# Optimization experiments

Hardware: AMD Instinct MI355X
Metric: run time of the kernel (lower is better)

Reference implementation:

```python
import jax, jax.numpy as jnp
import numpy as np

B, N, D, H, F = 16, 512, 768, 12, 3072
HD = D // H
EPS = 1e-5
NEG_INF = -1e30  # stand-in for -inf; softmax of all -inf rows handled via nan_to_num semantics


def layer_norm(x, g, b):
    mu = jnp.mean(x, axis=-1, keepdims=True)
    var = jnp.mean(jnp.square(x - mu), axis=-1, keepdims=True)
    return (x - mu) * jax.lax.rsqrt(var + EPS) * g + b


def setup_inputs() -> dict:
    key = jax.random.key(0)
    ks = jax.random.split(key, 16)
    s = 0.02
    return {
        "x": jax.random.normal(ks[0], (B, N, D), jnp.float32),
        "spatial_encoding": jax.random.normal(ks[1], (B, N, N), jnp.float32),
        "edge_encoding": jax.random.normal(ks[2], (B, N, N), jnp.float32),
        "Wq": jax.random.normal(ks[3], (D, D), jnp.float32) * s,
        "Wk": jax.random.normal(ks[4], (D, D), jnp.float32) * s,
        "Wv": jax.random.normal(ks[5], (D, D), jnp.float32) * s,
        "bv": jnp.zeros((D,), jnp.float32),
        "Wo": jax.random.normal(ks[6], (D, D), jnp.float32) * s,
        "bo": jnp.zeros((D,), jnp.float32),
        "g1": jnp.ones((D,), jnp.float32),
        "be1": jnp.zeros((D,), jnp.float32),
        "g2": jnp.ones((D,), jnp.float32),
        "be2": jnp.zeros((D,), jnp.float32),
        "W1": jax.random.normal(ks[7], (D, F), jnp.float32) * s,
        "bf1": jnp.zeros((F,), jnp.float32),
        "W2": jax.random.normal(ks[8], (F, D), jnp.float32) * s,
        "bf2": jnp.zeros((D,), jnp.float32),
    }


def reference(x, spatial_encoding, edge_encoding, Wq, Wk, Wv, bv, Wo, bo,
              g1, be1, g2, be2, W1, bf1, W2, bf2):
    scale = D ** (-0.5)
    h = layer_norm(x, g1, be1)                              # n1(x)
    bias = (spatial_encoding + edge_encoding)[:, None]      # [B,1,N,N]

    q = (h @ Wq).reshape(B, N, H, HD).transpose(0, 2, 1, 3)  # [B,H,N,hd]
    k = (h @ Wk).reshape(B, N, H, HD).transpose(0, 2, 1, 3)
    v = (h @ Wv + bv).reshape(B, N, H, HD).transpose(0, 2, 1, 3)

    a = jnp.einsum('bhqd,bhkd->bhqk', q, k) * scale + bias   # [B,H,N,N]
    # pad rows (all-zero score rows) get -inf -> softmax NaN -> nan_to_num -> 0
    row_nonzero = jnp.any(a != 0, axis=-1, keepdims=True)
    a = jnp.where(row_nonzero, a, NEG_INF)
    p = jax.nn.softmax(a, axis=-1)
    p = jnp.where(row_nonzero, p, 0.0)  # mirrors nan_to_num on all -inf rows

    o = jnp.einsum('bhqk,bhkd->bhqd', p, v)                  # [B,H,N,hd]
    o = o.transpose(0, 2, 1, 3).reshape(B, N, D)
    att_output = o @ Wo + bo + x                              # residual

    pad_mask = jnp.any(att_output == 0, axis=-1)              # [B,N]
    ffn_in = layer_norm(x, g2, be2)                           # note: n2(x), as in source
    hmid = jax.nn.gelu(ffn_in @ W1 + bf1, approximate=True)
    ffn_out = hmid @ W2 + bf2 + att_output
    return jnp.where(pad_mask[..., None], 0.0, ffn_out)
```

## Files before the change

### kernel.cpp

```cpp
#include <hip/hip_runtime.h>
#include <math.h>

typedef unsigned short u16;
typedef __bf16 bf16x8 __attribute__((ext_vector_type(8)));
typedef float f32x4 __attribute__((ext_vector_type(4)));

__device__ __forceinline__ u16 f2bf(float f){
  union{float f; unsigned u;} v; v.f = f;
  return (u16)((v.u + 0x7fffu + ((v.u >> 16) & 1u)) >> 16);
}
__device__ __forceinline__ float bf2f(u16 b){
  union{unsigned u; float f;} v; v.u = (unsigned)b << 16; return v.f;
}

#define LOG2E 1.4426950408889634f

__global__ void prep_weights(const float* __restrict__ Wq, const float* __restrict__ Wk,
                             const float* __restrict__ Wv, const float* __restrict__ Wo,
                             const float* __restrict__ W1, const float* __restrict__ W2,
                             const float* __restrict__ g1, const float* __restrict__ g2,
                             u16* __restrict__ WqkvT, u16* __restrict__ WoT,
                             u16* __restrict__ W1T, u16* __restrict__ W2T, float qscale){
  __shared__ float t[32][33];
  int bid = blockIdx.x;
  const float* src; u16* dst; const float* rs; float sc; int R, C, bx, by;
  if (bid < 576)      {            src=Wq; dst=WqkvT;          rs=g1;      sc=qscale; R=768;  C=768;  bx=bid%24; by=bid/24; }
  else if (bid <1152) { bid-=576;  src=Wk; dst=WqkvT+768*768;  rs=g1;      sc=1.f;    R=768;  C=768;  bx=bid%24; by=bid/24; }
  else if (bid <1728) { bid-=1152; src=Wv; dst=WqkvT+1536*768; rs=g1;      sc=1.f;    R=768;  C=768;  bx=bid%24; by=bid/24; }
  else if (bid <2304) { bid-=1728; src=Wo; dst=WoT;            rs=nullptr; sc=1.f;    R=768;  C=768;  bx=bid%24; by=bid/24; }
  else if (bid <4608) { bid-=2304; src=W1; dst=W1T;            rs=g2;      sc=1.f;    R=768;  C=3072; bx=bid%96; by=bid/96; }
  else                { bid-=4608; src=W2; dst=W2T;            rs=nullptr; sc=1.f;    R=3072; C=768;  bx=bid%24; by=bid/24; }
  int c0 = bx * 32, r0 = by * 32;
  int tx = threadIdx.x, ty = threadIdx.y;
  #pragma unroll
  for (int i = 0; i < 4; i++)
    t[ty + i*8][tx] = src[(size_t)(r0 + ty + i*8) * C + c0 + tx];
  __syncthreads();
  float fac = (rs ? rs[r0 + tx] : 1.f) * sc;
  #pragma unroll
  for (int i = 0; i < 4; i++)
    dst[(size_t)(c0 + ty + i*8) * R + r0 + tx] = f2bf(t[tx][ty + i*8] * fac);
}

__global__ __launch_bounds__(256) void fold_bias(
    const float* __restrict__ Wq, const float* __restrict__ Wk,
    const float* __restrict__ Wv, const float* __restrict__ W1,
    const float* __restrict__ be1, const float* __restrict__ be2,
    const float* __restrict__ bv, const float* __restrict__ bf1,
    float* __restrict__ qkvb, float* __restrict__ bf1f){
  __shared__ float red[4][64];
  int tx = threadIdx.x & 63, ty = threadIdx.x >> 6;
  int j = blockIdx.x * 64 + tx;
  const float* W; int col, stride; const float* bvec;
  if (j < 768)       { W = Wq; col = j;        stride = 768;  bvec = be1; }
  else if (j < 1536) { W = Wk; col = j - 768;  stride = 768;  bvec = be1; }
  else if (j < 2304) { W = Wv; col = j - 1536; stride = 768;  bvec = be1; }
  else               { W = W1; col = j - 2304; stride = 3072; bvec = be2; }
  float s = 0.f;
  for (int k = ty * 192; k < (ty + 1) * 192; k++)
    s += bvec[k] * W[(size_t)k * stride + col];
  red[ty][tx] = s;
  __syncthreads();
  if (ty == 0){
    s = red[0][tx] + red[1][tx] + red[2][tx] + red[3][tx];
    if (j < 1536)      qkvb[j] = s;
    else if (j < 2304) qkvb[j] = s + bv[col];
    else               bf1f[col] = s + bf1[col];
  }
}

__global__ void bias_prep(u16* __restrict__ dst, const float* __restrict__ sp,
                          const float* __restrict__ ed){
  int t = blockIdx.x * blockDim.x + threadIdx.x;
  int row = t >> 7, c0 = (t & 127) * 4;
  size_t base = (size_t)row * 512;
  float4 s = *(const float4*)&sp[base + c0];
  float4 e = *(const float4*)&ed[base + c0];
  int kt = c0 >> 7, cw = c0 & 127, fk = cw >> 4, l0 = cw & 15;
  u16* o = dst + base + kt*128 + fk;
  o[(l0+0)*8] = f2bf((s.x+e.x)*LOG2E);
  o[(l0+1)*8] = f2bf((s.y+e.y)*LOG2E);
  o[(l0+2)*8] = f2bf((s.z+e.z)*LOG2E);
  o[(l0+3)*8] = f2bf((s.w+e.w)*LOG2E);
}

__global__ __launch_bounds__(256) void ln_kernel(
    const float* __restrict__ x, u16* __restrict__ hn){
  const int lane = threadIdx.x & 63, wave = threadIdx.x >> 6;
  const int row = blockIdx.x * 4 + wave;
  const float4* xr = (const float4*)(x + (size_t)row * 768);
  float4 v[3];
  float sum = 0.f, sq = 0.f;
  #pragma unroll
  for (int c = 0; c < 3; c++){
    v[c] = xr[lane + 64*c];
    sum += v[c].x + v[c].y + v[c].z + v[c].w;
    sq  += v[c].x*v[c].x + v[c].y*v[c].y + v[c].z*v[c].z + v[c].w*v[c].w;
  }
  #pragma unroll
  for (int d = 1; d < 64; d <<= 1){ sum += __shfl_xor(sum, d); sq += __shfl_xor(sq, d); }
  float mu  = sum * (1.f/768.f);
  float var = sq * (1.f/768.f) - mu*mu;
  float rs  = rsqrtf(var + 1e-5f);
  #pragma unroll
  for (int c = 0; c < 3; c++){
    int f4 = lane + 64*c;
    ushort4 o{f2bf((v[c].x-mu)*rs), f2bf((v[c].y-mu)*rs),
              f2bf((v[c].z-mu)*rs), f2bf((v[c].w-mu)*rs)};
    ((ushort4*)(hn + (size_t)row*768))[f4] = o;
  }
}

template<int EPI>
__global__ __launch_bounds__(256, 2) void gemm_bt(
    const u16* __restrict__ A, const u16* __restrict__ Bt, void* __restrict__ Cout,
    const float* __restrict__ bias, const void* __restrict__ resid,
    u16* __restrict__ vt, int M, int Nn, int K){
  __shared__ __align__(16) u16 As[128*64];
  __shared__ __align__(16) u16 Bs[128*64];
  const int tid = threadIdx.x, lane = tid & 63, wave = tid >> 6;
  const int wm = wave >> 1, wn = wave & 1;
  const int l15 = lane & 15, lg = lane >> 4;
  const int bid = blockIdx.y * gridDim.x + blockIdx.x;
  const int cpx = (gridDim.x * gridDim.y) >> 3;
  const int swz = (bid & 7) * cpx + (bid >> 3);
  const int m0 = (swz / gridDim.x) * 128, n0 = (swz % gridDim.x) * 128;
  f32x4 acc[4][4] = {};
  for (int k0 = 0; k0 < K; k0 += 64){
    #pragma unroll
    for (int i = 0; i < 4; i++){
      int chunk = i*256 + tid;
      int row = chunk >> 3, seg = (chunk & 7) ^ (row & 7);
      __builtin_amdgcn_global_load_lds(
        (const __attribute__((address_space(1))) void*)&A[(size_t)(m0+row)*K + k0 + seg*8],
        (__attribute__((address_space(3))) void*)&As[(size_t)(i*256 + wave*64)*8], 16, 0, 0);
      __builtin_amdgcn_global_load_lds(
        (const __attribute__((address_space(1))) void*)&Bt[(size_t)(n0+row)*K + k0 + seg*8],
        (__attribute__((address_space(3))) void*)&Bs[(size_t)(i*256 + wave*64)*8], 16, 0, 0);
    }
    __syncthreads();
    bf16x8 af[4][2], bfr[4][2];
    #pragma unroll
    for (int i = 0; i < 4; i++){
      int ra = wm*64 + i*16 + l15, rb = wn*64 + i*16 + l15;
      #pragma unroll
      for (int kk = 0; kk < 2; kk++){
        af[i][kk]  = *(const bf16x8*)&As[ra*64 + (((kk*4 + lg) ^ (l15 & 7)) << 3)];
        bfr[i][kk] = *(const bf16x8*)&Bs[rb*64 + (((kk*4 + lg) ^ (l15 & 7)) << 3)];
      }
    }
    #pragma unroll
    for (int kk = 0; kk < 2; kk++)
      #pragma unroll
      for (int i = 0; i < 4; i++)
        #pragma unroll
        for (int j = 0; j < 4; j++)
          acc[i][j] = __builtin_amdgcn_mfma_f32_16x16x32_bf16(af[i][kk], bfr[j][kk], acc[i][j], 0, 0, 0);
    __syncthreads();
  }
  #pragma unroll
  for (int i = 0; i < 4; i++){
    int row_base = m0 + wm*64 + i*16 + lg*4;
    #pragma unroll
    for (int j = 0; j < 4; j++){
      int col = n0 + wn*64 + j*16 + l15;
      float bcol = bias ? bias[col] : 0.f;
      if (EPI == 5 && col >= 1536){
        int hv = (col - 1536) >> 6, hd = (col - 1536) & 63;
        int b = row_base >> 9, n = row_base & 511;
        int within = n & 127;
        int newn = (n & ~127) + ((((within >> 3) ^ (hd & 7)) << 3)) + (within & 7);
        ushort4 ov{f2bf(acc[i][j][0] + bcol), f2bf(acc[i][j][1] + bcol),
                   f2bf(acc[i][j][2] + bcol), f2bf(acc[i][j][3] + bcol)};
        *(ushort4*)&vt[(((size_t)(b*12 + hv)*64 + hd) << 9) + newn] = ov;
        continue;
      }
      #pragma unroll
      for (int r = 0; r < 4; r++){
        size_t idx = (size_t)(row_base + r) * Nn + col;
        float v = acc[i][j][r] + bcol;
        if (EPI == 3){
          v += ((const float*)resid)[idx];
          ((u16*)Cout)[idx] = f2bf(v);
        } else if (EPI == 4){
          v += bf2f(((const u16*)resid)[idx]);
          ((float*)Cout)[idx] = v;
        } else if (EPI == 2){
          float u = v + 0.044715f * v * v * v;
          float e = exp2f(-2.3022182f * u);
          ((u16*)Cout)[idx] = f2bf(v * __builtin_amdgcn_rcpf(1.f + e));
        } else {
          ((u16*)Cout)[idx] = f2bf(v);
        }
      }
    }
  }
}

__global__ __launch_bounds__(256, 2) void attn_kernel(
    const u16* __restrict__ qkv, const u16* __restrict__ VTg,
    const u16* __restrict__ biasPb, u16* __restrict__ Og){
  __shared__ __align__(16) u16 Ks[128*64];
  __shared__ __align__(16) u16 Vs[64*128];
  __shared__ __align__(16) u16 Pl[4*32*136];
  const int tid = threadIdx.x, lane = tid & 63, wave = tid >> 6;
  const int l15 = lane & 15, lg = lane >> 4;
  const int bid = blockIdx.y * 4 + blockIdx.x;
  const int swz = (bid & 7) * 96 + (bid >> 3);
  const int bh = swz >> 2, b = bh / 12, h = bh % 12;
  const int q0 = (swz & 3) * 128 + wave * 32;
  const u16* Qb = qkv + (size_t)b * 512 * 2304 + h * 64;
  const u16* Kb = Qb + 768;
  const u16* Vbh = VTg + (size_t)bh * 64 * 512;
  u16* Pw = &Pl[wave * 32 * 136];

  bf16x8 qf[2][2];
  #pragma unroll
  for (int fm = 0; fm < 2; fm++)
    #pragma unroll
    for (int kk = 0; kk < 2; kk++)
      qf[fm][kk] = *(const bf16x8*)&Qb[(size_t)(q0 + fm*16 + l15)*2304 + kk*32 + lg*8];

  f32x4 O[2][4] = {};
  float lrow[2][4] = {};

  for (int kt = 0; kt < 4; kt++){
    const int k0 = kt * 128;
    bf16x8 bb[2][4];
    #pragma unroll
    for (int fm = 0; fm < 2; fm++)
      #pragma unroll
      for (int r = 0; r < 4; r++){
        int qrow = q0 + fm*16 + lg*4 + r;
        bb[fm][r] = *(const bf16x8*)&biasPb[((size_t)(b*512 + qrow)*4 + kt)*128 + l15*8];
      }
    #pragma unroll
    for (int i = 0; i < 4; i++){
      int chunk = i*256 + tid;
      int r = chunk >> 3, cc = chunk & 7;
      __builtin_amdgcn_global_load_lds(
        (const __attribute__((address_space(1))) void*)&Kb[(size_t)(k0 + r)*2304 + ((cc ^ (r & 7)) << 3)],
        (__attribute__((address_space(3))) void*)&Ks[(size_t)(i*256 + wave*64)*8],
        16, 0, 0);
    }
    #pragma unroll
    for (int i = 0; i < 4; i++){
      int chunk = i*256 + tid;
      int r = chunk >> 4, cc = chunk & 15;
      __builtin_amdgcn_global_load_lds(
        (const __attribute__((address_space(1))) void*)&Vbh[(size_t)r*512 + k0 + (cc << 3)],
        (__attribute__((address_space(3))) void*)&Vs[(size_t)(i*256 + wave*64)*8],
        16, 0, 0);
    }
    __syncthreads();

    f32x4 S[2][8] = {};
    #pragma unroll
    for (int fk = 0; fk < 8; fk++)
      #pragma unroll
      for (int kk = 0; kk < 2; kk++){
        int row = fk*16 + l15;
        bf16x8 kf = *(const bf16x8*)&Ks[row*64 + (((kk*4 + lg) ^ (l15 & 7)) << 3)];
        S[0][fk] = __builtin_amdgcn_mfma_f32_16x16x32_bf16(qf[0][kk], kf, S[0][fk], 0,0,0);
        S[1][fk] = __builtin_amdgcn_mfma_f32_16x16x32_bf16(qf[1][kk], kf, S[1][fk], 0,0,0);
      }
    #pragma unroll
    for (int fm = 0; fm < 2; fm++)
      #pragma unroll
      for (int r = 0; r < 4; r++){
        float rs = 0.f;
        #pragma unroll
        for (int fk = 0; fk < 8; fk++){
          float p = exp2f(S[fm][fk][r] + (float)bb[fm][r][fk]);
          S[fm][fk][r] = p;
          rs += p;
        }
        rs += __shfl_xor(rs, 1); rs += __shfl_xor(rs, 2);
        rs += __shfl_xor(rs, 4); rs += __shfl_xor(rs, 8);
        lrow[fm][r] += rs;
      }
    #pragma unroll
    for (int fm = 0; fm < 2; fm++)
      #pragma unroll
      for (int fk = 0; fk < 8; fk++)
        #pragma unroll
        for (int r = 0; r < 4; r++)
          Pw[(fm*16 + lg*4 + r)*136 + fk*16 + l15] = f2bf(S[fm][fk][r]);
    bf16x8 pf[2][4];
    #pragma unroll
    for (int fm = 0; fm < 2; fm++)
      #pragma unroll
      for (int kk = 0; kk < 4; kk++)
        pf[fm][kk] = *(const bf16x8*)&Pw[(fm*16 + l15)*136 + kk*32 + lg*8];
    #pragma unroll
    for (int fn = 0; fn < 4; fn++)
      #pragma unroll
      for (int kk = 0; kk < 4; kk++){
        int row = fn*16 + l15;
        bf16x8 vf = *(const bf16x8*)&Vs[row*128 + (((kk*4 + lg) ^ (l15 & 7)) << 3)];
        O[0][fn] = __builtin_amdgcn_mfma_f32_16x16x32_bf16(pf[0][kk], vf, O[0][fn], 0,0,0);
        O[1][fn] = __builtin_amdgcn_mfma_f32_16x16x32_bf16(pf[1][kk], vf, O[1][fn], 0,0,0);
      }
    __syncthreads();
  }
  #pragma unroll
  for (int fm = 0; fm < 2; fm++)
    #pragma unroll
    for (int r = 0; r < 4; r++){
      float inv = __builtin_amdgcn_rcpf(lrow[fm][r]);
      int qrow = q0 + fm*16 + lg*4 + r;
      #pragma unroll
      for (int fn = 0; fn < 4; fn++)
        Og[((size_t)b*512 + qrow)*768 + h*64 + fn*16 + l15] = f2bf(O[fm][fn][r] * inv);
    }
}

extern "C" void kernel_launch(void* const* d_in, const int* in_sizes, int n_in,
                              void* d_out, int out_size, void* d_ws, size_t ws_size,
                              hipStream_t stream){
  const float* x   = (const float*)d_in[0];
  const float* sp  = (const float*)d_in[1];
  const float* ed  = (const float*)d_in[2];
  const float* Wq  = (const float*)d_in[3];
  const float* Wk  = (const float*)d_in[4];
  const float* Wv  = (const float*)d_in[5];
  const float* bv  = (const float*)d_in[6];
  const float* Wo  = (const float*)d_in[7];
  const float* bo  = (const float*)d_in[8];
  const float* g1  = (const float*)d_in[9];
  const float* be1 = (const float*)d_in[10];
  const float* g2  = (const float*)d_in[11];
  const float* be2 = (const float*)d_in[12];
  const float* W1  = (const float*)d_in[13];
  const float* bf1 = (const float*)d_in[14];
  const float* W2  = (const float*)d_in[15];
  const float* bf2 = (const float*)d_in[16];

  char* w = (char*)d_ws;
  size_t off = 0;
  auto alloc = [&](size_t bytes)->void*{ void* p = w + off; off += (bytes + 255) & ~(size_t)255; return p; };
  u16*   Gg    = (u16*)  alloc(8192ull*3072*2);
  u16*   qkv   = Gg;
  u16*   VTg   = (u16*)  alloc(8192ull*768*2);
  u16*   hn    = (u16*)  alloc(8192ull*768*2);
  u16*   Og    = (u16*)  alloc(8192ull*768*2);
  u16*   attb  = (u16*)  alloc(8192ull*768*2);
  u16*   biasPb= (u16*)  alloc(16ull*512*512*2);
  u16*   WqkvT = (u16*)  alloc(2304ull*768*2);
  u16*   WoT   = (u16*)  alloc(768ull*768*2);
  u16*   W1T   = (u16*)  alloc(3072ull*768*2);
  u16*   W2T   = (u16*)  alloc(768ull*3072*2);
  float* qkvb  = (float*)alloc(2304ull*4);
  float* bf1f  = (float*)alloc(3072ull*4);

  const float qscale = 0.03608439182435161f * LOG2E;

  prep_weights<<<6912, dim3(32,8), 0, stream>>>(Wq, Wk, Wv, Wo, W1, W2, g1, g2,
                                                WqkvT, WoT, W1T, W2T, qscale);
  fold_bias<<<84, 256, 0, stream>>>(Wq, Wk, Wv, W1, be1, be2, bv, bf1, qkvb, bf1f);
  bias_prep<<<4096, 256, 0, stream>>>(biasPb, sp, ed);

  ln_kernel<<<2048, 256, 0, stream>>>(x, hn);

  gemm_bt<5><<<dim3(18,64),256,0,stream>>>(hn, WqkvT, qkv, qkvb, nullptr, VTg, 8192, 2304, 768);

  attn_kernel<<<dim3(4,192),256,0,stream>>>(qkv, VTg, biasPb, Og);

  gemm_bt<3><<<dim3(6,64),256,0,stream>>>(Og, WoT, attb, bo, x, nullptr, 8192, 768, 768);

  gemm_bt<2><<<dim3(24,64),256,0,stream>>>(hn, W1T, Gg, bf1f, nullptr, nullptr, 8192, 3072, 768);
  gemm_bt<4><<<dim3(6,64),256,0,stream>>>(Gg, W2T, (float*)d_out, bf2, attb, nullptr, 8192, 768, 3072);
}
```

Measured before the change: 256.8 us.

## Merge attention and FFN1 GEMM into one interleaved launch

Combines the attention kernel and the first FFN GEMM into a single launch whose blocks are interleaved one attention tile per two GEMM tiles. Both stages depend only on earlier outputs, so they can share the GPU and overlap memory-bound and MFMA-bound work. This also removes one kernel launch. Buffers are reorganized (qkv gets its own allocation, attb reuses it) so the GEMM output Gg no longer aliases qkv. In exchange, shared memory is sized for the larger of the two bodies, which may change occupancy, and the uniform block mix could cause tail imbalance.

Result: no change. 255.3 us (-0.6%).

```diff
diff --git a/kernel.cpp b/kernel.cpp
--- a/kernel.cpp
+++ b/kernel.cpp
@@ -197,15 +197,14 @@
   }
 }
 
-__global__ __launch_bounds__(256, 2) void attn_kernel(
-    const u16* __restrict__ qkv, const u16* __restrict__ VTg,
+__device__ __forceinline__ void attn_body(
+    int bid, u16* sm, const u16* __restrict__ qkv, const u16* __restrict__ VTg,
     const u16* __restrict__ biasPb, u16* __restrict__ Og){
-  __shared__ __align__(16) u16 Ks[128*64];
-  __shared__ __align__(16) u16 Vs[64*128];
-  __shared__ __align__(16) u16 Pl[4*32*136];
+  u16* Ks = sm;
+  u16* Vs = sm + 8192;
+  u16* Pl = sm + 16384;
   const int tid = threadIdx.x, lane = tid & 63, wave = tid >> 6;
   const int l15 = lane & 15, lg = lane >> 4;
-  const int bid = blockIdx.y * 4 + blockIdx.x;
   const int swz = (bid & 7) * 96 + (bid >> 3);
   const int bh = swz >> 2, b = bh / 12, h = bh % 12;
   const int q0 = (swz & 3) * 128 + wave * 32;
@@ -313,6 +312,81 @@
       for (int fn = 0; fn < 4; fn++)
         Og[((size_t)b*512 + qrow)*768 + h*64 + fn*16 + l15] = f2bf(O[fm][fn][r] * inv);
     }
+}
+
+__device__ __forceinline__ void ffn1_body(
+    int fid, u16* sm, const u16* __restrict__ A, const u16* __restrict__ Bt,
+    u16* __restrict__ Cout, const float* __restrict__ bias){
+  u16* As = sm;
+  u16* Bs = sm + 8192;
+  const int Nn = 3072, K = 768;
+  const int tid = threadIdx.x, lane = tid & 63, wave = tid >> 6;
+  const int wm = wave >> 1, wn = wave & 1;
+  const int l15 = lane & 15, lg = lane >> 4;
+  const int swz = (fid & 7) * 192 + (fid >> 3);
+  const int m0 = (swz / 24) * 128, n0 = (swz % 24) * 128;
+  f32x4 acc[4][4] = {};
+  for (int k0 = 0; k0 < K; k0 += 64){
+    #pragma unroll
+    for (int i = 0; i < 4; i++){
+      int chunk = i*256 + tid;
+      int row = chunk >> 3, seg = (chunk & 7) ^ (row & 7);
+      __builtin_amdgcn_global_load_lds(
+        (const __attribute__((address_space(1))) void*)&A[(size_t)(m0+row)*K + k0 + seg*8],
+        (__attribute__((address_space(3))) void*)&As[(size_t)(i*256 + wave*64)*8], 16, 0, 0);
+      __builtin_amdgcn_global_load_lds(
+        (const __attribute__((address_space(1))) void*)&Bt[(size_t)(n0+row)*K + k0 + seg*8],
+        (__attribute__((address_space(3))) void*)&Bs[(size_t)(i*256 + wave*64)*8], 16, 0, 0);
+    }
+    __syncthreads();
+    bf16x8 af[4][2], bfr[4][2];
+    #pragma unroll
+    for (int i = 0; i < 4; i++){
+      int ra = wm*64 + i*16 + l15, rb = wn*64 + i*16 + l15;
+      #pragma unroll
+      for (int kk = 0; kk < 2; kk++){
+        af[i][kk]  = *(const bf16x8*)&As[ra*64 + (((kk*4 + lg) ^ (l15 & 7)) << 3)];
+        bfr[i][kk] = *(const bf16x8*)&Bs[rb*64 + (((kk*4 + lg) ^ (l15 & 7)) << 3)];
+      }
+    }
+    #pragma unroll
+    for (int kk = 0; kk < 2; kk++)
+      #pragma unroll
+      for (int i = 0; i < 4; i++)
+        #pragma unroll
+        for (int j = 0; j < 4; j++)
+          acc[i][j] = __builtin_amdgcn_mfma_f32_16x16x32_bf16(af[i][kk], bfr[j][kk], acc[i][j], 0, 0, 0);
+    __syncthreads();
+  }
+  #pragma unroll
+  for (int i = 0; i < 4; i++){
+    int row_base = m0 + wm*64 + i*16 + lg*4;
+    #pragma unroll
+    for (int j = 0; j < 4; j++){
+      int col = n0 + wn*64 + j*16 + l15;
+      float bcol = bias[col];
+      #pragma unroll
+      for (int r = 0; r < 4; r++){
+        size_t idx = (size_t)(row_base + r) * Nn + col;
+        float v = acc[i][j][r] + bcol;
+        float u = v + 0.044715f * v * v * v;
+        float e = exp2f(-2.3022182f * u);
+        Cout[idx] = f2bf(v * __builtin_amdgcn_rcpf(1.f + e));
+      }
+    }
+  }
+}
+
+__global__ __launch_bounds__(256, 2) void attn_ffn1(
+    const u16* __restrict__ qkv, const u16* __restrict__ VTg,
+    const u16* __restrict__ biasPb, u16* __restrict__ Og,
+    const u16* __restrict__ hn, const u16* __restrict__ W1T,
+    u16* __restrict__ Gg, const float* __restrict__ bf1f){
+  __shared__ __align__(16) u16 sm[33792];
+  const int bid = blockIdx.x;
+  const int t = bid / 3, r = bid - t * 3;
+  if (r == 0) attn_body(t, sm, qkv, VTg, biasPb, Og);
+  else        ffn1_body(2*t + (r-1), sm, hn, W1T, Gg, bf1f);
 }
 
 extern "C" void kernel_launch(void* const* d_in, const int* in_sizes, int n_in,
@@ -340,11 +414,11 @@
   size_t off = 0;
   auto alloc = [&](size_t bytes)->void*{ void* p = w + off; off += (bytes + 255) & ~(size_t)255; return p; };
   u16*   Gg    = (u16*)  alloc(8192ull*3072*2);
-  u16*   qkv   = Gg;
+  u16*   qkv   = (u16*)  alloc(8192ull*2304*2);
+  u16*   attb  = qkv;
   u16*   VTg   = (u16*)  alloc(8192ull*768*2);
   u16*   hn    = (u16*)  alloc(8192ull*768*2);
   u16*   Og    = (u16*)  alloc(8192ull*768*2);
-  u16*   attb  = (u16*)  alloc(8192ull*768*2);
   u16*   biasPb= (u16*)  alloc(16ull*512*512*2);
   u16*   WqkvT = (u16*)  alloc(2304ull*768*2);
   u16*   WoT   = (u16*)  alloc(768ull*768*2);
@@ -364,10 +438,9 @@
 
   gemm_bt<5><<<dim3(18,64),256,0,stream>>>(hn, WqkvT, qkv, qkvb, nullptr, VTg, 8192, 2304, 768);
 
-  attn_kernel<<<dim3(4,192),256,0,stream>>>(qkv, VTg, biasPb, Og);
+  attn_ffn1<<<2304, 256, 0, stream>>>(qkv, VTg, biasPb, Og, hn, W1T, Gg, bf1f);
 
   gemm_bt<3><<<dim3(6,64),256,0,stream>>>(Og, WoT, attb, bo, x, nullptr, 8192, 768, 768);
 
-  gemm_bt<2><<<dim3(24,64),256,0,stream>>>(hn, W1T, Gg, bf1f, nullptr, nullptr, 8192, 3072, 768);
   gemm_bt<4><<<dim3(6,64),256,0,stream>>>(Gg, W2T, (float*)d_out, bf2, attb, nullptr, 8192, 768, 3072);
 }
```
